# Optimization experiments

Measured on AMD Instinct MI355X. Metric: run time of the kernel, lower is better.

The kernel has to match this reference:

```python
import jax, jax.numpy as jnp
import numpy as np

NEG = -9999.0
PAD_IDX = 0
SOS_IDX = 47


def setup_inputs() -> dict:
    key = jax.random.key(0)
    k1, k2, k3 = jax.random.split(key, 3)
    B, T, S = 1024, 512, 48
    features = jax.random.normal(k1, (B, T, S), dtype=jnp.float32)
    states = jax.random.randint(k2, (B, T), 1, S - 1)  # avoid pad/sos as gold tags
    mask = jnp.ones((B, T), dtype=jnp.float32)
    # transition matrix ~ N(-1, 0.1) with CRF structural constraints (as in __init__)
    transition = -1.0 + 0.1 * jax.random.normal(k3, (S, S), dtype=jnp.float32)
    transition = transition.at[SOS_IDX, :].set(NEG)
    transition = transition.at[:, PAD_IDX].set(NEG)
    transition = transition.at[PAD_IDX, :].set(NEG)
    transition = transition.at[PAD_IDX, PAD_IDX].set(0.0)
    return {"features": features, "states": states, "mask": mask, "transition": transition}


def _numerator(features, states, mask, transition):
    # score of the gold path: sum_t mask_t * (emission_t + transition[y_t, y_{t-1}])
    B = states.shape[0]
    sos_col = jnp.full((B, 1), SOS_IDX, dtype=states.dtype)
    states_ext = jnp.concatenate([sos_col, states], axis=1)  # [B, T+1]
    emis = jnp.take_along_axis(features, states[..., None], axis=2)[..., 0]  # [B, T]
    trans = transition[states_ext[:, 1:], states_ext[:, :-1]]  # [B, T]
    return jnp.sum((emis + trans) * mask, axis=1)  # [B]


def _denominator(features, mask, transition):
    # CRF forward algorithm: log-partition via log-sum-exp scan over time
    B, T, S = features.shape
    init = jnp.full((B, S), NEG, dtype=features.dtype).at[:, SOS_IDX].set(0.0)

    def step(score, xs):
        emis_t, mask_t = xs  # [B, S], [B]
        # new[b, i] = lse_j( score[b, j] + emis[b, i] + transition[i, j] )
        new = jax.nn.logsumexp(
            score[:, None, :] + emis_t[:, :, None] + transition[None, :, :], axis=-1
        )
        m = mask_t[:, None]
        return new * m + score * (1.0 - m), None

    final, _ = jax.lax.scan(
        step, init, (jnp.swapaxes(features, 0, 1), jnp.swapaxes(mask, 0, 1))
    )
    return jax.nn.logsumexp(final, axis=-1)  # [B]


def reference(features, states, mask, transition):
    numer = _numerator(features, states, mask, transition)
    denom = _denominator(features, mask, transition)
    # per-sequence negative log-likelihood (denominator - numerator)
    return denom - numer
```

## Files before the change

### kernel.cpp

```cpp
#include <hip/hip_runtime.h>
#include <math.h>

#define B 1024
#define T 512
#define S 48
#define SOS 47

typedef _Float16 half2v __attribute__((ext_vector_type(2)));
typedef _Float16 half8v __attribute__((ext_vector_type(8)));

__device__ __forceinline__ float rdlane1(float v) {
    return __int_as_float(__builtin_amdgcn_readlane(__float_as_int(v), 1));
}

__global__ __launch_bounds__(64)
__attribute__((amdgpu_waves_per_eu(1, 1)))
void crf_fused(const float* __restrict__ feat,
               const int* __restrict__ states,
               const float* __restrict__ mask,
               const float* __restrict__ trans,
               float* __restrict__ out) {
    __shared__ __align__(16) _Float16 qbuf[2][64];
    __shared__ unsigned long long mbits[T / 64];
    const int b = blockIdx.x;
    const int lane = threadIdx.x;
    const int elane = (lane < S) ? lane : 0;
    const float* f_b = feat + (size_t)b * T * S;
    const float* m_b = mask + b * T;
    const int* st_b = states + b * T;

    float nsum = 0.f;
#pragma unroll
    for (int k2 = 0; k2 < T / 64; ++k2) {
        const int t = lane + k2 * 64;
        const int st = st_b[t];
        const int pv = (t == 0) ? SOS : st_b[t - 1];
        const float m = m_b[t];
        nsum += (f_b[t * S + st] + trans[st * S + pv]) * m;
        const unsigned long long bal = __ballot(m != 0.f);
        if (lane == 0) mbits[k2] = bal;
    }

    half2v eT[S / 2];
    {
        const float4* t4 = (const float4*)(trans + elane * S);
#pragma unroll
        for (int j4 = 0; j4 < S / 4; ++j4) {
            const float4 tv = t4[j4];
            const float e0 = (lane < S) ? __expf(tv.x) : 0.f;
            const float e1 = (lane < S) ? __expf(tv.y) : 0.f;
            const float e2 = (lane < S) ? __expf(tv.z) : 0.f;
            const float e3 = (lane < S) ? __expf(tv.w) : 0.f;
            eT[2 * j4 + 0] = half2v{(_Float16)e0, (_Float16)e1};
            eT[2 * j4 + 1] = half2v{(_Float16)e2, (_Float16)e3};
        }
    }

    float q = (lane == SOS) ? 1.f : 0.f;
    qbuf[0][lane] = (_Float16)q;
    float P = 1.f;
    int cexp = 0;

    float ering[2][8];
#pragma unroll
    for (int k = 0; k < 8; ++k)
        ering[0][k] = f_b[k * S + elane];

#pragma unroll 1
    for (int tb = 0; tb < T / 8; ++tb) {
        const int pbk = tb & 1;
        const int tn = ((tb + 1) & (T / 8 - 1)) * 8;
#pragma unroll
        for (int k = 0; k < 8; ++k)
            ering[pbk ^ 1][k] = f_b[(tn + k) * S + elane];
        const unsigned int mbyte =
            ((const volatile unsigned char*)mbits)[tb];
#pragma unroll
        for (int k = 0; k < 8; ++k) {
            asm volatile("" ::: "memory");
            const float E = __expf(ering[pbk][k]);
            const half8v* qb = (const half8v*)&qbuf[k & 1][0];
            float ax = 0.f, ay = 0.f, az = 0.f, aw = 0.f;
#pragma unroll
            for (int c = 0; c < 6; ++c) {
                const half8v h = qb[c];
                const half2v p0 = __builtin_shufflevector(h, h, 0, 1);
                const half2v p1 = __builtin_shufflevector(h, h, 2, 3);
                const half2v p2 = __builtin_shufflevector(h, h, 4, 5);
                const half2v p3 = __builtin_shufflevector(h, h, 6, 7);
                ax = __builtin_amdgcn_fdot2(eT[4 * c + 0], p0, ax, false);
                ay = __builtin_amdgcn_fdot2(eT[4 * c + 1], p1, ay, false);
                az = __builtin_amdgcn_fdot2(eT[4 * c + 2], p2, az, false);
                aw = __builtin_amdgcn_fdot2(eT[4 * c + 3], p3, aw, false);
            }
            const float d = (ax + ay) + (az + aw);
            const float t = d * E;
            const float t1 = rdlane1(t);
            const float r = __builtin_amdgcn_rcpf(t1);
            const float qn = t * r;
            const bool live = ((mbyte >> k) & 1u) != 0u;
            q = live ? qn : q;
            qbuf[(k + 1) & 1][lane] = (_Float16)q;
            const float f = live ? r : 1.f;
            P *= f;
            const int pbits = __float_as_int(P);
            cexp += (pbits >> 23) - 127;
            P = __int_as_float((pbits & 0x007FFFFF) | 0x3F800000);
        }
    }

    float ps = q;
#pragma unroll
    for (int off = 32; off > 0; off >>= 1) {
        ps += __shfl_xor(ps, off, 64);
        nsum += __shfl_xor(nsum, off, 64);
    }
    if (lane == 0) {
        const float C = -((float)cexp * 0.69314718056f + __logf(P));
        out[b] = C + __logf(ps) - nsum;
    }
}

extern "C" void kernel_launch(void* const* d_in, const int* in_sizes, int n_in,
                              void* d_out, int out_size, void* d_ws, size_t ws_size,
                              hipStream_t stream) {
    const float* feat   = (const float*)d_in[0];
    const int*   states = (const int*)d_in[1];
    const float* mask   = (const float*)d_in[2];
    const float* trans  = (const float*)d_in[3];
    float* out = (float*)d_out;

    crf_fused<<<dim3(B), dim3(64), 0, stream>>>(feat, states, mask, trans, out);
}
```

Before: 310.3 us.

## Interleave four CRF sequences per wavefront to hide the serial recurrence latency

Each 64-lane block now handles four batch sequences instead of one, interleaving their forward recurrences step by step. The goal is instruction-level parallelism across the long dependent chain of each step (LDS round trip, dot products, readlane, reciprocal). The normaliser is also restructured so the readlane of the emission is taken and exponentiated ahead of the dot product, which shortens that chain. The grid drops to a quarter as many blocks, so with one wave per SIMD far fewer SIMDs are busy, and each wave carries four times the per-step instruction count and more register and LDS state.

```diff
diff --git a/kernel.cpp b/kernel.cpp
--- a/kernel.cpp
+++ b/kernel.cpp
@@ -5,6 +5,8 @@
 #define T 512
 #define S 48
 #define SOS 47
+#define TS (T * S)
+#define R 4
 
 typedef _Float16 half2v __attribute__((ext_vector_type(2)));
 typedef _Float16 half8v __attribute__((ext_vector_type(8)));
@@ -15,30 +17,35 @@
 
 __global__ __launch_bounds__(64)
 __attribute__((amdgpu_waves_per_eu(1, 1)))
-void crf_fused(const float* __restrict__ feat,
-               const int* __restrict__ states,
-               const float* __restrict__ mask,
-               const float* __restrict__ trans,
+void crf_fused(const float* __restrict__ feat, const int* __restrict__ states,
+               const float* __restrict__ mask, const float* __restrict__ trans,
                float* __restrict__ out) {
-    __shared__ __align__(16) _Float16 qbuf[2][64];
-    __shared__ unsigned long long mbits[T / 64];
-    const int b = blockIdx.x;
+    __shared__ __align__(16) _Float16 qbuf[R][2][64];
+    __shared__ unsigned long long mbits[R][T / 64];
     const int lane = threadIdx.x;
     const int elane = (lane < S) ? lane : 0;
-    const float* f_b = feat + (size_t)b * T * S;
-    const float* m_b = mask + b * T;
-    const int* st_b = states + b * T;
+    const int b0 = blockIdx.x * R;
 
-    float nsum = 0.f;
+    float nsum[R];
 #pragma unroll
-    for (int k2 = 0; k2 < T / 64; ++k2) {
-        const int t = lane + k2 * 64;
-        const int st = st_b[t];
-        const int pv = (t == 0) ? SOS : st_b[t - 1];
-        const float m = m_b[t];
-        nsum += (f_b[t * S + st] + trans[st * S + pv]) * m;
-        const unsigned long long bal = __ballot(m != 0.f);
-        if (lane == 0) mbits[k2] = bal;
+    for (int r = 0; r < R; ++r) {
+        const float* fr = feat + (size_t)(b0 + r) * TS;
+        const int* str = states + (b0 + r) * T;
+        const float* mr = mask + (b0 + r) * T;
+        float acc = 0.f;
+#pragma unroll
+        for (int k2 = 0; k2 < T / 64; ++k2) {
+            const int t = lane + 64 * k2;
+            const int st = str[t];
+            const int pv = (t == 0) ? SOS : str[t - 1];
+            const float m = mr[t];
+            acc += (fr[t * S + st] + trans[st * S + pv]) * m;
+            const unsigned long long bal = __ballot(m != 0.f);
+            if (lane == 0) mbits[r][k2] = bal;
+        }
+#pragma unroll
+        for (int off = 32; off > 0; off >>= 1) acc += __shfl_xor(acc, off, 64);
+        nsum[r] = acc;
     }
 
     half2v eT[S / 2];
@@ -56,68 +63,85 @@
         }
     }
 
-    float q = (lane == SOS) ? 1.f : 0.f;
-    qbuf[0][lane] = (_Float16)q;
-    float P = 1.f;
-    int cexp = 0;
+    float q[R], P[R];
+    int cexp[R];
+    const float* frp[R];
+#pragma unroll
+    for (int r = 0; r < R; ++r) {
+        q[r] = (lane == SOS) ? 1.f : 0.f;
+        qbuf[r][0][lane] = (_Float16)q[r];
+        P[r] = 1.f;
+        cexp[r] = 0;
+        frp[r] = feat + (size_t)(b0 + r) * TS + elane;
+    }
 
-    float ering[2][8];
+    float ering[R][8];
 #pragma unroll
-    for (int k = 0; k < 8; ++k)
-        ering[0][k] = f_b[k * S + elane];
+    for (int r = 0; r < R; ++r)
+#pragma unroll
+        for (int k = 0; k < 8; ++k) ering[r][k] = frp[r][k * S];
 
 #pragma unroll 1
     for (int tb = 0; tb < T / 8; ++tb) {
-        const int pbk = tb & 1;
-        const int tn = ((tb + 1) & (T / 8 - 1)) * 8;
+        unsigned mby[R];
 #pragma unroll
-        for (int k = 0; k < 8; ++k)
-            ering[pbk ^ 1][k] = f_b[(tn + k) * S + elane];
-        const unsigned int mbyte =
-            ((const volatile unsigned char*)mbits)[tb];
+        for (int r = 0; r < R; ++r)
+            mby[r] = ((const unsigned char*)&mbits[r][0])[tb];
 #pragma unroll
         for (int k = 0; k < 8; ++k) {
-            asm volatile("" ::: "memory");
-            const float E = __expf(ering[pbk][k]);
-            const half8v* qb = (const half8v*)&qbuf[k & 1][0];
-            float ax = 0.f, ay = 0.f, az = 0.f, aw = 0.f;
+            const int t = tb * 8 + k;
+            const int tp = (t + 8) & (T - 1);
+            float E[R], E1[R], d[R];
 #pragma unroll
-            for (int c = 0; c < 6; ++c) {
-                const half8v h = qb[c];
-                const half2v p0 = __builtin_shufflevector(h, h, 0, 1);
-                const half2v p1 = __builtin_shufflevector(h, h, 2, 3);
-                const half2v p2 = __builtin_shufflevector(h, h, 4, 5);
-                const half2v p3 = __builtin_shufflevector(h, h, 6, 7);
-                ax = __builtin_amdgcn_fdot2(eT[4 * c + 0], p0, ax, false);
-                ay = __builtin_amdgcn_fdot2(eT[4 * c + 1], p1, ay, false);
-                az = __builtin_amdgcn_fdot2(eT[4 * c + 2], p2, az, false);
-                aw = __builtin_amdgcn_fdot2(eT[4 * c + 3], p3, aw, false);
+            for (int r = 0; r < R; ++r) {
+                const float emis = ering[r][k];
+                E[r] = __expf(emis);
+                E1[r] = __expf(rdlane1(emis));
+                ering[r][k] = frp[r][tp * S];
             }
-            const float d = (ax + ay) + (az + aw);
-            const float t = d * E;
-            const float t1 = rdlane1(t);
-            const float r = __builtin_amdgcn_rcpf(t1);
-            const float qn = t * r;
-            const bool live = ((mbyte >> k) & 1u) != 0u;
-            q = live ? qn : q;
-            qbuf[(k + 1) & 1][lane] = (_Float16)q;
-            const float f = live ? r : 1.f;
-            P *= f;
-            const int pbits = __float_as_int(P);
-            cexp += (pbits >> 23) - 127;
-            P = __int_as_float((pbits & 0x007FFFFF) | 0x3F800000);
+#pragma unroll
+            for (int r = 0; r < R; ++r) {
+                const half8v* qb = (const half8v*)&qbuf[r][k & 1][0];
+                float ax = 0.f, ay = 0.f, az = 0.f, aw = 0.f;
+#pragma unroll
+                for (int c = 0; c < 6; ++c) {
+                    const half8v h = qb[c];
+                    const half2v p0 = __builtin_shufflevector(h, h, 0, 1);
+                    const half2v p1 = __builtin_shufflevector(h, h, 2, 3);
+                    const half2v p2 = __builtin_shufflevector(h, h, 4, 5);
+                    const half2v p3 = __builtin_shufflevector(h, h, 6, 7);
+                    ax = __builtin_amdgcn_fdot2(eT[4 * c + 0], p0, ax, false);
+                    ay = __builtin_amdgcn_fdot2(eT[4 * c + 1], p1, ay, false);
+                    az = __builtin_amdgcn_fdot2(eT[4 * c + 2], p2, az, false);
+                    aw = __builtin_amdgcn_fdot2(eT[4 * c + 3], p3, aw, false);
+                }
+                d[r] = (ax + ay) + (az + aw);
+            }
+#pragma unroll
+            for (int r = 0; r < R; ++r) {
+                const float t1 = rdlane1(d[r]) * E1[r];
+                const float rc = __builtin_amdgcn_rcpf(t1);
+                const float qn = (d[r] * E[r]) * rc;
+                const bool live = ((mby[r] >> k) & 1u) != 0u;
+                q[r] = live ? qn : q[r];
+                qbuf[r][(k + 1) & 1][lane] = (_Float16)q[r];
+                P[r] *= live ? rc : 1.f;
+                const int pb = __float_as_int(P[r]);
+                cexp[r] += (pb >> 23) - 127;
+                P[r] = __int_as_float((pb & 0x007FFFFF) | 0x3F800000);
+            }
         }
     }
 
-    float ps = q;
 #pragma unroll
-    for (int off = 32; off > 0; off >>= 1) {
-        ps += __shfl_xor(ps, off, 64);
-        nsum += __shfl_xor(nsum, off, 64);
-    }
-    if (lane == 0) {
-        const float C = -((float)cexp * 0.69314718056f + __logf(P));
-        out[b] = C + __logf(ps) - nsum;
+    for (int r = 0; r < R; ++r) {
+        float ps = q[r];
+#pragma unroll
+        for (int off = 32; off > 0; off >>= 1) ps += __shfl_xor(ps, off, 64);
+        if (lane == 0) {
+            const float C = -((float)cexp[r] * 0.69314718056f + __logf(P[r]));
+            out[b0 + r] = C + __logf(ps) - nsum[r];
+        }
     }
 }
 
@@ -130,5 +154,5 @@
     const float* trans  = (const float*)d_in[3];
     float* out = (float*)d_out;
 
-    crf_fused<<<dim3(B), dim3(64), 0, stream>>>(feat, states, mask, trans, out);
+    crf_fused<<<dim3(B / R), dim3(64), 0, stream>>>(feat, states, mask, trans, out);
 }
```

Result: slower. 433.0 us (+39.5%).
